# Optimization experiments

Hardware: AMD Instinct MI355X
Metric: run time of the kernel (lower is better)

The kernel has to match this reference:

```python
import jax, jax.numpy as jnp
import numpy as np

B, T, HID = 2, 1024, 1024
H, DK, DV = 16, 64, 64
K = 4            # short conv kernel size
CG = 15          # CG iterations (max_cg_step_training)
EPS = 1e-5       # norm_eps


def setup_inputs() -> dict:
    key = jax.random.key(0)
    ks = jax.random.split(key, 12)
    s = 1.0 / np.sqrt(HID)
    nrm = lambda k, sh, sc: (jax.random.normal(k, sh, jnp.float32) * sc)
    hidden_states = nrm(ks[0], (B, T, HID), 1.0)
    Wq = nrm(ks[1], (HID, HID), s)
    Wk = nrm(ks[2], (HID, HID), s)
    Wv = nrm(ks[3], (HID, HID), s)
    Wa = nrm(ks[4], (HID, H), s)
    Wb = nrm(ks[5], (HID, H), s)
    bb = jnp.zeros((H,), jnp.float32)
    A_log = jnp.log(jax.random.uniform(ks[6], (H,), jnp.float32, 1e-3, 16.0))
    dt = jnp.exp(jax.random.uniform(ks[7], (H,), jnp.float32) * (np.log(0.1) - np.log(0.001)) + np.log(0.001))
    dt = jnp.clip(dt, 1e-4)
    dt_bias = dt + jnp.log(-jnp.expm1(-dt))
    lam_init = float(np.log(np.exp(1.0 - 0.25) - 1.0))
    lambda_params = jnp.full((HID,), lam_init, jnp.float32)
    Wconv_q = nrm(ks[8], (HID, K), 0.3)
    Wconv_k = nrm(ks[9], (HID, K), 0.3)
    norm_w = jnp.ones((DV,), jnp.float32)
    Wo = nrm(ks[10], (HID, HID), s)
    return dict(hidden_states=hidden_states, Wq=Wq, Wk=Wk, Wv=Wv, Wa=Wa, Wb=Wb, bb=bb,
                A_log=A_log, dt_bias=dt_bias, lambda_params=lambda_params,
                Wconv_q=Wconv_q, Wconv_k=Wconv_k, norm_w=norm_w, Wo=Wo)


def _short_conv(x, w):
    # causal depthwise conv1d + silu. x: [b,t,c], w: [c,K]
    t = x.shape[1]
    xp = jnp.pad(x, ((0, 0), (K - 1, 0), (0, 0)))
    y = sum(xp[:, i:i + t, :] * w[:, i] for i in range(K))
    return jax.nn.silu(y)


def _l2norm(x):
    return x * jax.lax.rsqrt(jnp.sum(x * x, -1, keepdims=True) + 1e-6)


def _forward(hidden_states, Wq, Wk, Wv, Wa, Wb, bb, A_log, dt_bias, lambda_params, Wconv_q, Wconv_k, norm_w, Wo):
    b, t, _ = hidden_states.shape
    q = _short_conv(hidden_states @ Wq, Wconv_q)
    k = _short_conv(hidden_states @ Wk, Wconv_k)
    v = hidden_states @ Wv
    q = _l2norm(q.reshape(b, t, H, DK))
    k = _l2norm(k.reshape(b, t, H, DK))
    v = v.reshape(b, t, H, DV)
    beta = jax.nn.sigmoid(hidden_states @ Wb + bb)                         # [b,t,h]
    g = -jnp.exp(A_log) * jax.nn.softplus(hidden_states @ Wa + dt_bias)    # [b,t,h]
    lamb = jax.nn.softplus(lambda_params).reshape(H, DK) + 0.25            # [h,dk]

    def cg_solve(Hkk, rhs):
        # solve (Hkk + diag(lamb)) x = rhs, fixed-iteration CG, batched over [b,h]
        mv = lambda p: jnp.einsum('bhij,bhj->bhi', Hkk, p) + lamb * p
        x = jnp.zeros_like(rhs)
        r = rhs
        p = r
        rs = jnp.sum(r * r, -1, keepdims=True)
        for _ in range(CG):
            Ap = mv(p)
            alpha = rs / (jnp.sum(p * Ap, -1, keepdims=True) + 1e-12)
            x = x + alpha * p
            r = r - alpha * Ap
            rs_new = jnp.sum(r * r, -1, keepdims=True)
            p = r + (rs_new / (rs + 1e-12)) * p
            rs = rs_new
        return x

    def step(carry, inp):
        Hkk, Hkv = carry
        qt, kt, vt, gt, bt = inp
        decay = jnp.exp(gt)[..., None, None]
        w = bt[..., None, None]
        Hkk = decay * Hkk + w * (kt[..., :, None] * kt[..., None, :])
        Hkv = decay * Hkv + w * (kt[..., :, None] * vt[..., None, :])
        x = cg_solve(Hkk, qt)
        o = jnp.einsum('bhi,bhij->bhj', x, Hkv)
        return (Hkk, Hkv), o

    qT = q.transpose(1, 0, 2, 3)
    kT = k.transpose(1, 0, 2, 3)
    vT = v.transpose(1, 0, 2, 3)
    gT = g.transpose(1, 0, 2)
    bT = beta.transpose(1, 0, 2)
    Hkk0 = jnp.zeros((b, H, DK, DK), hidden_states.dtype)
    Hkv0 = jnp.zeros((b, H, DK, DV), hidden_states.dtype)
    _, oT = jax.lax.scan(jax.checkpoint(step), (Hkk0, Hkv0), (qT, kT, vT, gT, bT))
    o = oT.transpose(1, 0, 2, 3)                                           # [b,t,h,dv]
    o = o * jax.lax.rsqrt(jnp.mean(o * o, -1, keepdims=True) + EPS) * norm_w
    return o.reshape(b, t, H * DV) @ Wo


def reference(hidden_states, Wq, Wk, Wv, Wa, Wb, bb, A_log, dt_bias, lambda_params, Wconv_q, Wconv_k, norm_w, Wo):
    return _forward(hidden_states, Wq, Wk, Wv, Wa, Wb, bb, A_log, dt_bias, lambda_params, Wconv_q, Wconv_k, norm_w, Wo)
```

## Files before the change

### kernel.cpp

```cpp
#include <hip/hip_runtime.h>
#include <hip/hip_bf16.h>
#include <stdint.h>

#define T_LEN 1024
#define HIDN  1024
#define NH    16
#define DKV   64
#define KCONV 4
#define CG_IT 15
#define CC    32
#define NC    (T_LEN / CC)
#define PAD   68

typedef __attribute__((ext_vector_type(8))) short          bf16x8;
typedef __attribute__((ext_vector_type(8))) unsigned short u16x8;
typedef __attribute__((ext_vector_type(4))) unsigned short u16x4;
typedef __attribute__((ext_vector_type(4))) float          f32x4;

__device__ __forceinline__ float softplusf(float x) {
    return x > 20.f ? x : log1pf(expf(x));
}
__device__ __forceinline__ unsigned short f2bf(float x) {
    __hip_bfloat16 b = __float2bfloat16(x);
    return *reinterpret_cast<unsigned short*>(&b);
}
__device__ __forceinline__ bf16x8 pack8(float4 a, float4 b) {
    union { bf16x8 v; unsigned short u[8]; } r;
    r.u[0] = f2bf(a.x); r.u[1] = f2bf(a.y); r.u[2] = f2bf(a.z); r.u[3] = f2bf(a.w);
    r.u[4] = f2bf(b.x); r.u[5] = f2bf(b.y); r.u[6] = f2bf(b.z); r.u[7] = f2bf(b.w);
    return r.v;
}

__global__ __launch_bounds__(256) void prep(const float* __restrict__ hidden,
                                            const float* __restrict__ Wq,
                                            const float* __restrict__ Wk,
                                            const float* __restrict__ Wv,
                                            const float* __restrict__ Wo,
                                            unsigned short* __restrict__ hidden_bf,
                                            unsigned short* __restrict__ WqkvT,
                                            unsigned short* __restrict__ WoT)
{
    __shared__ unsigned short sT[64][68];
    int blk = blockIdx.x;
    int tid = threadIdx.x;
    if (blk < 2048) {
        int i = blk * 256 + tid;
        float4 v = *reinterpret_cast<const float4*>(hidden + (size_t)i * 4);
        u16x4 o;
        o.x = f2bf(v.x); o.y = f2bf(v.y); o.z = f2bf(v.z); o.w = f2bf(v.w);
        *reinterpret_cast<u16x4*>(hidden_bf + (size_t)i * 4) = o;
        return;
    }
    int r = blk - 2048;
    int m = r >> 8;
    int local = r & 255;
    int n0 = (local & 15) * 64, k0 = (local >> 4) * 64;
    const float* W = (m == 0) ? Wq : (m == 1) ? Wk : (m == 2) ? Wv : Wo;
    unsigned short* WT = (m < 3) ? (WqkvT + (size_t)m * HIDN * HIDN) : WoT;

    int rr = tid >> 4, cc4 = (tid & 15) * 4;
#pragma unroll
    for (int p = 0; p < 4; p++) {
        int rw = p * 16 + rr;
        float4 v = *reinterpret_cast<const float4*>(&W[(size_t)(k0 + rw) * HIDN + n0 + cc4]);
        sT[cc4 + 0][rw] = f2bf(v.x);
        sT[cc4 + 1][rw] = f2bf(v.y);
        sT[cc4 + 2][rw] = f2bf(v.z);
        sT[cc4 + 3][rw] = f2bf(v.w);
    }
    __syncthreads();
#pragma unroll
    for (int p = 0; p < 4; p++) {
        int rw = p * 16 + rr;
        u16x4 v = *reinterpret_cast<const u16x4*>(&sT[rw][cc4]);
        *reinterpret_cast<u16x4*>(&WT[(size_t)(n0 + rw) * HIDN + k0 + cc4]) = v;
    }
}

__global__ __launch_bounds__(256) void proj_gb(const float* __restrict__ hidden,
                                               const float* __restrict__ Wa,
                                               const float* __restrict__ Wb,
                                               const float* __restrict__ bb,
                                               const float* __restrict__ A_log,
                                               const float* __restrict__ dt_bias,
                                               float* __restrict__ g_out,
                                               float* __restrict__ beta_out)
{
    int wvid = threadIdx.x >> 6, lane = threadIdx.x & 63;
    int row = blockIdx.x * 4 + wvid;
    const float* hr = hidden + (size_t)row * HIDN;

    float da[16], db[16];
#pragma unroll
    for (int h = 0; h < 16; h++) { da[h] = 0.f; db[h] = 0.f; }

#pragma unroll 4
    for (int j = 0; j < 16; j++) {
        int i = j * 64 + lane;
        float x = hr[i];
        const float4* wa4 = reinterpret_cast<const float4*>(Wa + (size_t)i * NH);
        const float4* wb4 = reinterpret_cast<const float4*>(Wb + (size_t)i * NH);
#pragma unroll
        for (int q = 0; q < 4; q++) {
            float4 wa = wa4[q], wb = wb4[q];
            da[q * 4 + 0] += x * wa.x; da[q * 4 + 1] += x * wa.y;
            da[q * 4 + 2] += x * wa.z; da[q * 4 + 3] += x * wa.w;
            db[q * 4 + 0] += x * wb.x; db[q * 4 + 1] += x * wb.y;
            db[q * 4 + 2] += x * wb.z; db[q * 4 + 3] += x * wb.w;
        }
    }
#pragma unroll
    for (int m = 1; m < 64; m <<= 1) {
#pragma unroll
        for (int h = 0; h < 16; h++) {
            da[h] += __shfl_xor(da[h], m);
            db[h] += __shfl_xor(db[h], m);
        }
    }
    float dah = 0.f, dbh = 0.f;
#pragma unroll
    for (int h = 0; h < 16; h++) {
        bool sel = (lane == h);
        dah = sel ? da[h] : dah;
        dbh = sel ? db[h] : dbh;
    }
    if (lane < 16) {
        float sp = softplusf(dah + dt_bias[lane]);
        g_out[row * NH + lane]    = -expf(A_log[lane]) * sp;
        beta_out[row * NH + lane] = 1.f / (1.f + expf(-(dbh + bb[lane])));
    }
}

__global__ __launch_bounds__(256) void gemm_bf16(const unsigned short* __restrict__ A,
                                                 const unsigned short* __restrict__ Bt,
                                                 float* __restrict__ C,
                                                 int M, int N, int K)
{
    __shared__ unsigned short sA[64][40];
    __shared__ unsigned short sB[64][40];
    const int tid = threadIdx.x;
    const int bm = blockIdx.y * 64, bn = blockIdx.x * 64;
    const int w = tid >> 6, lane = tid & 63;
    const int l16 = lane & 15, quad = lane >> 4;
    const int lrow = tid >> 2, lk = (tid & 3) * 8;

    f32x4 acc[4];
#pragma unroll
    for (int f = 0; f < 4; f++) acc[f] = (f32x4){0.f, 0.f, 0.f, 0.f};

    const size_t arow = (size_t)(bm + lrow) * K;
    const size_t brow = (size_t)(bn + lrow) * K;

    for (int k0 = 0; k0 < K; k0 += 32) {
        u16x8 av = *reinterpret_cast<const u16x8*>(A + arow + k0 + lk);
        u16x8 bv = *reinterpret_cast<const u16x8*>(Bt + brow + k0 + lk);
        *reinterpret_cast<u16x8*>(&sA[lrow][lk]) = av;
        *reinterpret_cast<u16x8*>(&sB[lrow][lk]) = bv;
        __syncthreads();

        bf16x8 aF = *reinterpret_cast<const bf16x8*>(&sA[w * 16 + l16][quad * 8]);
#pragma unroll
        for (int f = 0; f < 4; f++) {
            bf16x8 bF = *reinterpret_cast<const bf16x8*>(&sB[f * 16 + l16][quad * 8]);
            acc[f] = __builtin_amdgcn_mfma_f32_16x16x32_bf16(aF, bF, acc[f], 0, 0, 0);
        }
        __syncthreads();
    }

#pragma unroll
    for (int f = 0; f < 4; f++) {
#pragma unroll
        for (int i = 0; i < 4; i++) {
            int m = bm + w * 16 + quad * 4 + i;
            C[(size_t)m * N + bn + f * 16 + l16] = acc[f][i];
        }
    }
}

__global__ __launch_bounds__(256) void gemm_qkv128(const unsigned short* __restrict__ A,
                                                   const unsigned short* __restrict__ Bt,
                                                   float* __restrict__ C)
{
    const int K = 1024;
    __shared__ unsigned short sA[128][40];
    __shared__ unsigned short sB[128][40];
    const int tid = threadIdx.x;
    const int bm = blockIdx.y * 128;
    const int bn = blockIdx.x * 128;
    const int w = tid >> 6, lane = tid & 63;
    const int l16 = lane & 15, quad = lane >> 4;
    const int wm = (w >> 1) * 64, wn = (w & 1) * 64;
    const int lrow = tid >> 1, lk = (tid & 1) * 16;

    f32x4 acc[4][4];
#pragma unroll
    for (int i = 0; i < 4; i++)
#pragma unroll
        for (int f = 0; f < 4; f++) acc[i][f] = (f32x4){0.f, 0.f, 0.f, 0.f};

    const size_t arow = (size_t)(bm + lrow) * K + lk;
    const size_t brow = (size_t)(bn + lrow) * K + lk;

    for (int k0 = 0; k0 < K; k0 += 32) {
        u16x8 a0 = *reinterpret_cast<const u16x8*>(A + arow + k0);
        u16x8 a1 = *reinterpret_cast<const u16x8*>(A + arow + k0 + 8);
        u16x8 b0 = *reinterpret_cast<const u16x8*>(Bt + brow + k0);
        u16x8 b1 = *reinterpret_cast<const u16x8*>(Bt + brow + k0 + 8);
        *reinterpret_cast<u16x8*>(&sA[lrow][lk])     = a0;
        *reinterpret_cast<u16x8*>(&sA[lrow][lk + 8]) = a1;
        *reinterpret_cast<u16x8*>(&sB[lrow][lk])     = b0;
        *reinterpret_cast<u16x8*>(&sB[lrow][lk + 8]) = b1;
        __syncthreads();

        bf16x8 af[4], bf[4];
#pragma unroll
        for (int i = 0; i < 4; i++)
            af[i] = *reinterpret_cast<const bf16x8*>(&sA[wm + 16 * i + l16][8 * quad]);
#pragma unroll
        for (int f = 0; f < 4; f++)
            bf[f] = *reinterpret_cast<const bf16x8*>(&sB[wn + 16 * f + l16][8 * quad]);
#pragma unroll
        for (int i = 0; i < 4; i++)
#pragma unroll
            for (int f = 0; f < 4; f++)
                acc[i][f] = __builtin_amdgcn_mfma_f32_16x16x32_bf16(af[i], bf[f], acc[i][f], 0, 0, 0);
        __syncthreads();
    }

#pragma unroll
    for (int i = 0; i < 4; i++) {
#pragma unroll
        for (int f = 0; f < 4; f++) {
            int ncol = bn + wn + 16 * f + l16;
            int mat = ncol >> 10, nc = ncol & 1023;
            float* Cb = C + (size_t)mat * (2048u * 1024u) + nc;
            int mrow = bm + wm + 16 * i + 4 * quad;
#pragma unroll
            for (int reg = 0; reg < 4; reg++)
                Cb[(size_t)(mrow + reg) * 1024] = acc[i][f][reg];
        }
    }
}

__global__ __launch_bounds__(256) void cumsum_g(const float* __restrict__ g_in,
                                                const float* __restrict__ beta_in,
                                                float* __restrict__ G_out,
                                                float* __restrict__ betaT)
{
    __shared__ float wtot[4];
    int bh = blockIdx.x;
    int b = bh >> 4, h = bh & 15;
    int tid = threadIdx.x;
    int wv = tid >> 6, lane = tid & 63;
    int t4 = tid * 4;
    size_t src = ((size_t)(b * T_LEN) + t4) * NH + h;
    float g0 = g_in[src], g1 = g_in[src + NH], g2 = g_in[src + 2 * NH], g3 = g_in[src + 3 * NH];
    float b0 = beta_in[src], b1 = beta_in[src + NH], b2 = beta_in[src + 2 * NH], b3 = beta_in[src + 3 * NH];
    float c1 = g0 + g1, c2 = c1 + g2, c3 = c2 + g3;
    float x = c3;
#pragma unroll
    for (int off = 1; off < 64; off <<= 1) {
        float y = __shfl_up(x, off);
        if (lane >= off) x += y;
    }
    float base = x - c3;
    if (lane == 63) wtot[wv] = x;
    __syncthreads();
    float woff = 0.f;
#pragma unroll
    for (int q = 0; q < 4; q++) woff += (q < wv) ? wtot[q] : 0.f;
    base += woff;
    size_t dst = (size_t)bh * T_LEN + t4;
    G_out[dst]     = base + g0;
    G_out[dst + 1] = base + c1;
    G_out[dst + 2] = base + c2;
    G_out[dst + 3] = base + c3;
    betaT[dst] = b0; betaT[dst + 1] = b1; betaT[dst + 2] = b2; betaT[dst + 3] = b3;
}

__global__ __launch_bounds__(256) void conv_silu_l2(const float* __restrict__ qpre,
                                                    const float* __restrict__ kpre,
                                                    const float* __restrict__ Wcq,
                                                    const float* __restrict__ Wck,
                                                    float* __restrict__ qbuf,
                                                    float* __restrict__ kbuf)
{
    int gidAll = blockIdx.x * 4 + (threadIdx.x >> 6);
    int which = gidAll >> 15;
    int gid = gidAll & 32767;
    const float* pre = which ? kpre : qpre;
    const float* Wc  = which ? Wck : Wcq;
    float* out       = which ? kbuf : qbuf;
    int lane = threadIdx.x & 63;
    int h = gid & 15;
    int t = (gid >> 4) & (T_LEN - 1);
    int b = gid >> 14;
    int c = h * DKV + lane;
    float acc = 0.f;
#pragma unroll
    for (int i = 0; i < KCONV; i++) {
        int ts = t - (KCONV - 1) + i;
        if (ts >= 0)
            acc += pre[((size_t)(b * T_LEN) + ts) * HIDN + c] * Wc[c * KCONV + i];
    }
    float y = acc / (1.f + expf(-acc));
    float ss = y * y;
#pragma unroll
    for (int m = 1; m < 64; m <<= 1) ss += __shfl_xor(ss, m);
    out[((size_t)(b * T_LEN) + t) * HIDN + c] = y * rsqrtf(ss + 1e-6f);
}

__global__ __launch_bounds__(256) void chunk_local(const float* __restrict__ kbuf,
                                                   const float* __restrict__ vbuf,
                                                   const float* __restrict__ G,
                                                   const float* __restrict__ betaT,
                                                   float* __restrict__ Akk,
                                                   float* __restrict__ AkvT)
{
    __shared__ float sK[CC][PAD];
    __shared__ float sV[CC][PAD];
    __shared__ float sW[CC];
    int bid = blockIdx.x;
    int half = bid & 1;
    int cidx = bid >> 1;
    int chunk = cidx & (NC - 1), bh = cidx >> 5;
    int b = bh >> 4, h = bh & 15;
    int tid = threadIdx.x;
    int i = half * 32 + (tid >> 3);
    int j0 = (tid & 7) * 8;
    int ls = tid >> 3, ld = (tid & 7) * 8;
    int t0 = chunk * CC;

    {
        size_t ga = (((size_t)(b * T_LEN) + t0 + ls) * NH + h) * 64 + ld;
        *reinterpret_cast<float4*>(&sK[ls][ld])     = *reinterpret_cast<const float4*>(&kbuf[ga]);
        *reinterpret_cast<float4*>(&sK[ls][ld + 4]) = *reinterpret_cast<const float4*>(&kbuf[ga + 4]);
        *reinterpret_cast<float4*>(&sV[ls][ld])     = *reinterpret_cast<const float4*>(&vbuf[ga]);
        *reinterpret_cast<float4*>(&sV[ls][ld + 4]) = *reinterpret_cast<const float4*>(&vbuf[ga + 4]);
        if (tid < CC) {
            float gv = G[(size_t)bh * T_LEN + t0 + tid];
            float bv = betaT[(size_t)bh * T_LEN + t0 + tid];
            float gend = __shfl(gv, 31);
            sW[tid] = expf(gend - gv) * bv;
        }
    }
    __syncthreads();

    float akk[8], akv[8];
#pragma unroll
    for (int j = 0; j < 8; j++) { akk[j] = 0.f; akv[j] = 0.f; }
#pragma unroll 4
    for (int s = 0; s < CC; s++) {
        float wk = sW[s] * sK[s][i];
        float wv = sW[s] * sV[s][i];
        float4 ka = *reinterpret_cast<const float4*>(&sK[s][j0]);
        float4 kb = *reinterpret_cast<const float4*>(&sK[s][j0 + 4]);
        akk[0] += wk * ka.x; akk[1] += wk * ka.y; akk[2] += wk * ka.z; akk[3] += wk * ka.w;
        akk[4] += wk * kb.x; akk[5] += wk * kb.y; akk[6] += wk * kb.z; akk[7] += wk * kb.w;
        akv[0] += wv * ka.x; akv[1] += wv * ka.y; akv[2] += wv * ka.z; akv[3] += wv * ka.w;
        akv[4] += wv * kb.x; akv[5] += wv * kb.y; akv[6] += wv * kb.z; akv[7] += wv * kb.w;
    }
    size_t ob = ((size_t)cidx * 64 + i) * 64 + j0;
    *reinterpret_cast<float4*>(&Akk[ob])      = make_float4(akk[0], akk[1], akk[2], akk[3]);
    *reinterpret_cast<float4*>(&Akk[ob + 4])  = make_float4(akk[4], akk[5], akk[6], akk[7]);
    *reinterpret_cast<float4*>(&AkvT[ob])     = make_float4(akv[0], akv[1], akv[2], akv[3]);
    *reinterpret_cast<float4*>(&AkvT[ob + 4]) = make_float4(akv[4], akv[5], akv[6], akv[7]);
}

__global__ __launch_bounds__(256) void chunk_prefix(const float* __restrict__ Akk,
                                                    float* __restrict__ HkvT,
                                                    const float* __restrict__ G,
                                                    unsigned short* __restrict__ Hkk_bf)
{
    __shared__ float sDec[NC];
    int blk = blockIdx.x;
    int bh = blk >> 3, sub = blk & 7;
    int tid = threadIdx.x;
    if (tid < NC)
        sDec[tid] = (tid > 0)
            ? expf(G[(size_t)bh * T_LEN + tid * CC + CC - 1] - G[(size_t)bh * T_LEN + tid * CC - 1])
            : 1.f;
    __syncthreads();
    int flat = sub * 256 + tid;
    int mat = flat >> 10, e4 = flat & 1023;
    float4 state = make_float4(0.f, 0.f, 0.f, 0.f);
    if (mat == 0) {
        const float* src = Akk + (size_t)bh * NC * 4096 + (size_t)e4 * 4;
        unsigned short* dst = Hkk_bf + (size_t)bh * NC * 4096 + (size_t)e4 * 4;
#pragma unroll 1
        for (int c0 = 0; c0 < NC; c0 += 4) {
            float4 av[4];
#pragma unroll
            for (int e = 0; e < 4; e++)
                av[e] = *reinterpret_cast<const float4*>(src + (size_t)(c0 + e) * 4096);
#pragma unroll
            for (int e = 0; e < 4; e++) {
                u16x4 o;
                o.x = f2bf(state.x); o.y = f2bf(state.y); o.z = f2bf(state.z); o.w = f2bf(state.w);
                *reinterpret_cast<u16x4*>(dst + (size_t)(c0 + e) * 4096) = o;
                float d = sDec[c0 + e];
                state.x = d * state.x + av[e].x;
                state.y = d * state.y + av[e].y;
                state.z = d * state.z + av[e].z;
                state.w = d * state.w + av[e].w;
            }
        }
    } else {
        float* base = HkvT + (size_t)bh * NC * 4096 + (size_t)e4 * 4;
#pragma unroll 1
        for (int c0 = 0; c0 < NC; c0 += 4) {
            float4 av[4];
#pragma unroll
            for (int e = 0; e < 4; e++)
                av[e] = *reinterpret_cast<const float4*>(base + (size_t)(c0 + e) * 4096);
#pragma unroll
            for (int e = 0; e < 4; e++) {
                *reinterpret_cast<float4*>(base + (size_t)(c0 + e) * 4096) = state;
                float d = sDec[c0 + e];
                state.x = d * state.x + av[e].x;
                state.y = d * state.y + av[e].y;
                state.z = d * state.z + av[e].z;
                state.w = d * state.w + av[e].w;
            }
        }
    }
}

__global__ __launch_bounds__(256, 2) void scan_mfma(
    const float* __restrict__ qbuf, const float* __restrict__ kbuf,
    const float* __restrict__ vbuf, const float* __restrict__ G,
    const float* __restrict__ betaT, const unsigned short* __restrict__ Hkk_bf,
    const float* __restrict__ HkvT0, const float* __restrict__ lambda_p,
    const float* __restrict__ norm_w, unsigned short* __restrict__ obf)
{
    __shared__ __align__(16) unsigned short sP[4][16][72];
    __shared__ __align__(16) unsigned short sM[4][16][40];

    const int tid = threadIdx.x;
    const int wv = tid >> 6, lane = tid & 63;
    const int quad = lane >> 4, l16 = lane & 15;
    const int W = blockIdx.x * 4 + wv;
    const int half = W & 1;
    const int cidx = W >> 1;
    const int bh = cidx >> 5, chunk = cidx & 31;
    const int b = bh >> 4, h = bh & 15;
    const int t0 = chunk * CC;
    const int rbofs = 16 * half + 4 * quad;
    unsigned short (*sPw)[72] = sP[wv];
    unsigned short (*sMw)[40] = sM[wv];

    const size_t rbase = ((size_t)(b * T_LEN + t0) * NH + h) * 64;
    const float* Gb = G + (size_t)bh * T_LEN + t0;
    const float* Bb = betaT + (size_t)bh * T_LEN + t0;
    const float Gprev = (chunk > 0) ? Gb[-1] : 0.f;

    float Gt[4], et[4];
#pragma unroll
    for (int reg = 0; reg < 4; reg++) {
        float g = Gb[rbofs + reg];
        Gt[reg] = g;
        et[reg] = expf(g - Gprev);
    }
    float Co[2][4];
#pragma unroll
    for (int sn = 0; sn < 2; sn++) {
        int s = 16 * sn + l16;
        float Gs = Gb[s], bts = Bb[s];
#pragma unroll
        for (int reg = 0; reg < 4; reg++) {
            int t = rbofs + reg;
            Co[sn][reg] = (s <= t) ? expf(Gt[reg] - Gs) * bts : 0.f;
        }
    }
    float lam[4], nw[4];
#pragma unroll
    for (int f = 0; f < 4; f++) {
        lam[f] = softplusf(lambda_p[h * 64 + 16 * f + l16]) + 0.25f;
        nw[f]  = norm_w[16 * f + l16];
    }

    bf16x8 Kb[2][2];
#pragma unroll
    for (int sn = 0; sn < 2; sn++) {
        const float* kr = kbuf + rbase + (size_t)(16 * sn + l16) * 1024;
#pragma unroll
        for (int ks = 0; ks < 2; ks++) {
            float4 a = *reinterpret_cast<const float4*>(kr + 8 * quad + 32 * ks);
            float4 c = *reinterpret_cast<const float4*>(kr + 8 * quad + 32 * ks + 4);
            Kb[sn][ks] = pack8(a, c);
        }
    }
    bf16x8 KTb[4];
#pragma unroll
    for (int f = 0; f < 4; f++) {
        union { bf16x8 v; unsigned short u[8]; } r;
#pragma unroll
        for (int j = 0; j < 8; j++)
            r.u[j] = f2bf(kbuf[rbase + (size_t)(8 * quad + j) * 1024 + 16 * f + l16]);
        KTb[f] = r.v;
    }
    const size_t hbase = ((size_t)(bh * NC) + chunk) * 4096;
    bf16x8 Hb[4][2];
#pragma unroll
    for (int f = 0; f < 4; f++) {
        const unsigned short* hr = Hkk_bf + hbase + (size_t)(16 * f + l16) * 64;
#pragma unroll
        for (int ks = 0; ks < 2; ks++)
            Hb[f][ks] = *reinterpret_cast<const bf16x8*>(hr + 8 * quad + 32 * ks);
    }

    f32x4 X[4], R[4], P[4];
    float rs8[4];
#pragma unroll
    for (int reg = 0; reg < 4; reg++) rs8[reg] = 0.f;
#pragma unroll
    for (int f = 0; f < 4; f++) {
#pragma unroll
        for (int reg = 0; reg < 4; reg++) {
            float q = qbuf[rbase + (size_t)(rbofs + reg) * 1024 + 16 * f + l16];
            P[f][reg] = q; R[f][reg] = q; X[f][reg] = 0.f;
            rs8[reg] += q * q;
        }
    }
#pragma unroll
    for (int reg = 0; reg < 4; reg++) {
        float v = rs8[reg];
        v += __shfl_xor(v, 1); v += __shfl_xor(v, 2);
        v += __shfl_xor(v, 4); v += __shfl_xor(v, 8);
        rs8[reg] = v;
    }

    const f32x4 zero4 = {0.f, 0.f, 0.f, 0.f};

#pragma unroll 1
    for (int it = 0; it < CG_IT; it++) {
#pragma unroll
        for (int reg = 0; reg < 4; reg++)
#pragma unroll
            for (int f = 0; f < 4; f++)
                sPw[4 * quad + reg][16 * f + l16] = f2bf(P[f][reg]);
        __threadfence_block();
        bf16x8 Pa[2];
#pragma unroll
        for (int ks = 0; ks < 2; ks++)
            Pa[ks] = *reinterpret_cast<const bf16x8*>(&sPw[l16][8 * quad + 32 * ks]);
        f32x4 D[2];
#pragma unroll
        for (int sn = 0; sn < 2; sn++) {
            f32x4 d = __builtin_amdgcn_mfma_f32_16x16x32_bf16(Pa[0], Kb[sn][0], zero4, 0, 0, 0);
            D[sn] = __builtin_amdgcn_mfma_f32_16x16x32_bf16(Pa[1], Kb[sn][1], d, 0, 0, 0);
        }
#pragma unroll
        for (int sn = 0; sn < 2; sn++)
#pragma unroll
            for (int reg = 0; reg < 4; reg++)
                sMw[4 * quad + reg][16 * sn + l16] = f2bf(Co[sn][reg] * D[sn][reg]);
        __threadfence_block();
        bf16x8 Ma = *reinterpret_cast<const bf16x8*>(&sMw[l16][8 * quad]);
        f32x4 AP[4], A2[4];
#pragma unroll
        for (int f = 0; f < 4; f++) {
            AP[f] = __builtin_amdgcn_mfma_f32_16x16x32_bf16(Ma, KTb[f], zero4, 0, 0, 0);
            f32x4 a = __builtin_amdgcn_mfma_f32_16x16x32_bf16(Pa[0], Hb[f][0], zero4, 0, 0, 0);
            A2[f] = __builtin_amdgcn_mfma_f32_16x16x32_bf16(Pa[1], Hb[f][1], a, 0, 0, 0);
        }
#pragma unroll
        for (int f = 0; f < 4; f++)
#pragma unroll
            for (int reg = 0; reg < 4; reg++)
                AP[f][reg] = lam[f] * P[f][reg] + AP[f][reg] + et[reg] * A2[f][reg];
        float alpha[4], rsn[4];
#pragma unroll
        for (int reg = 0; reg < 4; reg++) {
            float s = 0.f;
#pragma unroll
            for (int f = 0; f < 4; f++) s += P[f][reg] * AP[f][reg];
            s += __shfl_xor(s, 1); s += __shfl_xor(s, 2);
            s += __shfl_xor(s, 4); s += __shfl_xor(s, 8);
            alpha[reg] = rs8[reg] / (s + 1e-12f);
            rsn[reg] = 0.f;
        }
#pragma unroll
        for (int f = 0; f < 4; f++)
#pragma unroll
            for (int reg = 0; reg < 4; reg++) {
                X[f][reg] += alpha[reg] * P[f][reg];
                float rv = R[f][reg] - alpha[reg] * AP[f][reg];
                R[f][reg] = rv;
                rsn[reg] += rv * rv;
            }
#pragma unroll
        for (int reg = 0; reg < 4; reg++) {
            float v = rsn[reg];
            v += __shfl_xor(v, 1); v += __shfl_xor(v, 2);
            v += __shfl_xor(v, 4); v += __shfl_xor(v, 8);
            float btac = v / (rs8[reg] + 1e-12f);
            rs8[reg] = v;
#pragma unroll
            for (int f = 0; f < 4; f++)
                P[f][reg] = R[f][reg] + btac * P[f][reg];
        }
    }

#pragma unroll
    for (int reg = 0; reg < 4; reg++)
#pragma unroll
        for (int f = 0; f < 4; f++)
            sPw[4 * quad + reg][16 * f + l16] = f2bf(X[f][reg]);
    __threadfence_block();
    bf16x8 Xa[2];
#pragma unroll
    for (int ks = 0; ks < 2; ks++)
        Xa[ks] = *reinterpret_cast<const bf16x8*>(&sPw[l16][8 * quad + 32 * ks]);
    f32x4 Do[2];
#pragma unroll
    for (int sn = 0; sn < 2; sn++) {
        f32x4 d = __builtin_amdgcn_mfma_f32_16x16x32_bf16(Xa[0], Kb[sn][0], zero4, 0, 0, 0);
        Do[sn] = __builtin_amdgcn_mfma_f32_16x16x32_bf16(Xa[1], Kb[sn][1], d, 0, 0, 0);
    }
#pragma unroll
    for (int sn = 0; sn < 2; sn++)
#pragma unroll
        for (int reg = 0; reg < 4; reg++)
            sMw[4 * quad + reg][16 * sn + l16] = f2bf(Co[sn][reg] * Do[sn][reg]);
    __threadfence_block();
    bf16x8 Mo = *reinterpret_cast<const bf16x8*>(&sMw[l16][8 * quad]);
    bf16x8 Vb[4];
#pragma unroll
    for (int f = 0; f < 4; f++) {
        union { bf16x8 v; unsigned short u[8]; } r;
#pragma unroll
        for (int j = 0; j < 8; j++)
            r.u[j] = f2bf(vbuf[rbase + (size_t)(8 * quad + j) * 1024 + 16 * f + l16]);
        Vb[f] = r.v;
    }
    bf16x8 Hvb[4][2];
#pragma unroll
    for (int f = 0; f < 4; f++) {
        const float* hr = HkvT0 + hbase + (size_t)(16 * f + l16) * 64;
#pragma unroll
        for (int ks = 0; ks < 2; ks++) {
            float4 a = *reinterpret_cast<const float4*>(hr + 8 * quad + 32 * ks);
            float4 c = *reinterpret_cast<const float4*>(hr + 8 * quad + 32 * ks + 4);
            Hvb[f][ks] = pack8(a, c);
        }
    }
    f32x4 O[4];
#pragma unroll
    for (int f = 0; f < 4; f++) {
        f32x4 o1 = __builtin_amdgcn_mfma_f32_16x16x32_bf16(Mo, Vb[f], zero4, 0, 0, 0);
        f32x4 o2 = __builtin_amdgcn_mfma_f32_16x16x32_bf16(Xa[0], Hvb[f][0], zero4, 0, 0, 0);
        o2 = __builtin_amdgcn_mfma_f32_16x16x32_bf16(Xa[1], Hvb[f][1], o2, 0, 0, 0);
#pragma unroll
        for (int reg = 0; reg < 4; reg++)
            O[f][reg] = o1[reg] + et[reg] * o2[reg];
    }
#pragma unroll
    for (int reg = 0; reg < 4; reg++) {
        float s = 0.f;
#pragma unroll
        for (int f = 0; f < 4; f++) s += O[f][reg] * O[f][reg];
        s += __shfl_xor(s, 1); s += __shfl_xor(s, 2);
        s += __shfl_xor(s, 4); s += __shfl_xor(s, 8);
        float scale = rsqrtf(s * (1.f / 64.f) + 1e-5f);
        size_t orow = rbase + (size_t)(rbofs + reg) * 1024;
#pragma unroll
        for (int f = 0; f < 4; f++)
            obf[orow + 16 * f + l16] = f2bf(O[f][reg] * scale * nw[f]);
    }
}

extern "C" void kernel_launch(void* const* d_in, const int* in_sizes, int n_in,
                              void* d_out, int out_size, void* d_ws, size_t ws_size,
                              hipStream_t stream)
{
    const float* hidden   = (const float*)d_in[0];
    const float* Wq       = (const float*)d_in[1];
    const float* Wk       = (const float*)d_in[2];
    const float* Wv       = (const float*)d_in[3];
    const float* Wa       = (const float*)d_in[4];
    const float* Wb       = (const float*)d_in[5];
    const float* bb       = (const float*)d_in[6];
    const float* A_log    = (const float*)d_in[7];
    const float* dt_bias  = (const float*)d_in[8];
    const float* lambda_p = (const float*)d_in[9];
    const float* Wconv_q  = (const float*)d_in[10];
    const float* Wconv_k  = (const float*)d_in[11];
    const float* norm_w   = (const float*)d_in[12];
    const float* Wo       = (const float*)d_in[13];
    float* out = (float*)d_out;

    float* ws = (float*)d_ws;
    const size_t SZ_BIG = (size_t)2 * T_LEN * HIDN;
    float* qpre = ws;
    float* kpre = qpre + SZ_BIG;
    float* vbuf = kpre + SZ_BIG;
    float* qbuf = vbuf + SZ_BIG;
    float* kbuf = qbuf + SZ_BIG;
    float* gbuf = kbuf + SZ_BIG;
    float* bbuf = gbuf + 32768;
    float* Gbuf = bbuf + 32768;
    float* btT  = Gbuf + 32768;
    float* Akk  = btT + 32768;
    float* AkvT = Akk + (size_t)32 * NC * 4096;
    unsigned short* WoT = (unsigned short*)(AkvT + (size_t)32 * NC * 4096);

    unsigned short* hidden_bf = (unsigned short*)AkvT;
    unsigned short* WqkvT = (unsigned short*)Akk;
    unsigned short* obuf_bf = (unsigned short*)kpre;
    unsigned short* Hkk_bf = (unsigned short*)qpre;

    const int M = 2 * T_LEN;

    prep<<<3072, 256, 0, stream>>>(hidden, Wq, Wk, Wv, Wo, hidden_bf, WqkvT, WoT);
    proj_gb<<<M / 4, 256, 0, stream>>>(hidden, Wa, Wb, bb, A_log, dt_bias, gbuf, bbuf);

    dim3 gq(3 * HIDN / 128, M / 128);
    gemm_qkv128<<<gq, 256, 0, stream>>>(hidden_bf, WqkvT, qpre);
    cumsum_g<<<32, 256, 0, stream>>>(gbuf, bbuf, Gbuf, btT);
    conv_silu_l2<<<2 * M * NH / 4, 256, 0, stream>>>(qpre, kpre, Wconv_q, Wconv_k,
                                                     qbuf, kbuf);
    chunk_local<<<2048, 256, 0, stream>>>(kbuf, vbuf, Gbuf, btT, Akk, AkvT);
    chunk_prefix<<<256, 256, 0, stream>>>(Akk, AkvT, Gbuf, Hkk_bf);
    scan_mfma<<<512, 256, 0, stream>>>(qbuf, kbuf, vbuf, Gbuf, btT, Hkk_bf, AkvT,
                                       lambda_p, norm_w, obuf_bf);
    dim3 gg(HIDN / 64, M / 64);
    gemm_bf16<<<gg, 256, 0, stream>>>(obuf_bf, WoT, out, M, HIDN, HIDN);
}
```

Baseline: 251.0 us.

## Use DPP row reductions in CG scan and merge chunk_local half-blocks

Swaps the 16-lane shuffle-xor reductions in the CG scan kernel for a DPP-based reduction helper (quad_perm swaps plus row_shr 4 and row_shr 8 with bound_ctrl). It also makes each chunk_local block compute both 32-row halves of the 64x64 chunk matrices, which halves the grid and avoids loading the same K/V tile twice. The DPP path is meant to cut the ds_swizzle/permute latency on the serial CG loop. Using row_shr instead of xor masks means only some lanes hold the full row sum, so lanes that later read it may get partial sums. This is a correctness risk.

```diff
diff --git a/kernel.cpp b/kernel.cpp
--- a/kernel.cpp
+++ b/kernel.cpp
@@ -29,6 +29,15 @@
     r.u[0] = f2bf(a.x); r.u[1] = f2bf(a.y); r.u[2] = f2bf(a.z); r.u[3] = f2bf(a.w);
     r.u[4] = f2bf(b.x); r.u[5] = f2bf(b.y); r.u[6] = f2bf(b.z); r.u[7] = f2bf(b.w);
     return r.v;
+}
+
+__device__ __forceinline__ float wsum16(float x) {
+    union { float f; int i; } a, b;
+    a.f = x; b.i = __builtin_amdgcn_update_dpp(0, a.i, 0xB1, 0xF, 0xF, true); x += b.f;
+    a.f = x; b.i = __builtin_amdgcn_update_dpp(0, a.i, 0x4E, 0xF, 0xF, true); x += b.f;
+    a.f = x; b.i = __builtin_amdgcn_update_dpp(0, a.i, 0x124, 0xF, 0xF, true); x += b.f;
+    a.f = x; b.i = __builtin_amdgcn_update_dpp(0, a.i, 0x128, 0xF, 0xF, true); x += b.f;
+    return x;
 }
 
 __global__ __launch_bounds__(256) void prep(const float* __restrict__ hidden,
@@ -320,13 +329,11 @@
     __shared__ float sK[CC][PAD];
     __shared__ float sV[CC][PAD];
     __shared__ float sW[CC];
-    int bid = blockIdx.x;
-    int half = bid & 1;
-    int cidx = bid >> 1;
+    int cidx = blockIdx.x;
     int chunk = cidx & (NC - 1), bh = cidx >> 5;
     int b = bh >> 4, h = bh & 15;
     int tid = threadIdx.x;
-    int i = half * 32 + (tid >> 3);
+    int i = tid >> 3;
     int j0 = (tid & 7) * 8;
     int ls = tid >> 3, ld = (tid & 7) * 8;
     int t0 = chunk * CC;
@@ -346,25 +353,35 @@
     }
     __syncthreads();
 
-    float akk[8], akv[8];
-#pragma unroll
-    for (int j = 0; j < 8; j++) { akk[j] = 0.f; akv[j] = 0.f; }
+    float akk[2][8], akv[2][8];
+#pragma unroll
+    for (int e = 0; e < 2; e++)
+#pragma unroll
+        for (int j = 0; j < 8; j++) { akk[e][j] = 0.f; akv[e][j] = 0.f; }
 #pragma unroll 4
     for (int s = 0; s < CC; s++) {
-        float wk = sW[s] * sK[s][i];
-        float wv = sW[s] * sV[s][i];
+        float w = sW[s];
+        float wk0 = w * sK[s][i],      wv0 = w * sV[s][i];
+        float wk1 = w * sK[s][i + 32], wv1 = w * sV[s][i + 32];
         float4 ka = *reinterpret_cast<const float4*>(&sK[s][j0]);
         float4 kb = *reinterpret_cast<const float4*>(&sK[s][j0 + 4]);
-        akk[0] += wk * ka.x; akk[1] += wk * ka.y; akk[2] += wk * ka.z; akk[3] += wk * ka.w;
-        akk[4] += wk * kb.x; akk[5] += wk * kb.y; akk[6] += wk * kb.z; akk[7] += wk * kb.w;
-        akv[0] += wv * ka.x; akv[1] += wv * ka.y; akv[2] += wv * ka.z; akv[3] += wv * ka.w;
-        akv[4] += wv * kb.x; akv[5] += wv * kb.y; akv[6] += wv * kb.z; akv[7] += wv * kb.w;
-    }
-    size_t ob = ((size_t)cidx * 64 + i) * 64 + j0;
-    *reinterpret_cast<float4*>(&Akk[ob])      = make_float4(akk[0], akk[1], akk[2], akk[3]);
-    *reinterpret_cast<float4*>(&Akk[ob + 4])  = make_float4(akk[4], akk[5], akk[6], akk[7]);
-    *reinterpret_cast<float4*>(&AkvT[ob])     = make_float4(akv[0], akv[1], akv[2], akv[3]);
-    *reinterpret_cast<float4*>(&AkvT[ob + 4]) = make_float4(akv[4], akv[5], akv[6], akv[7]);
+        akk[0][0] += wk0 * ka.x; akk[0][1] += wk0 * ka.y; akk[0][2] += wk0 * ka.z; akk[0][3] += wk0 * ka.w;
+        akk[0][4] += wk0 * kb.x; akk[0][5] += wk0 * kb.y; akk[0][6] += wk0 * kb.z; akk[0][7] += wk0 * kb.w;
+        akk[1][0] += wk1 * ka.x; akk[1][1] += wk1 * ka.y; akk[1][2] += wk1 * ka.z; akk[1][3] += wk1 * ka.w;
+        akk[1][4] += wk1 * kb.x; akk[1][5] += wk1 * kb.y; akk[1][6] += wk1 * kb.z; akk[1][7] += wk1 * kb.w;
+        akv[0][0] += wv0 * ka.x; akv[0][1] += wv0 * ka.y; akv[0][2] += wv0 * ka.z; akv[0][3] += wv0 * ka.w;
+        akv[0][4] += wv0 * kb.x; akv[0][5] += wv0 * kb.y; akv[0][6] += wv0 * kb.z; akv[0][7] += wv0 * kb.w;
+        akv[1][0] += wv1 * ka.x; akv[1][1] += wv1 * ka.y; akv[1][2] += wv1 * ka.z; akv[1][3] += wv1 * ka.w;
+        akv[1][4] += wv1 * kb.x; akv[1][5] += wv1 * kb.y; akv[1][6] += wv1 * kb.z; akv[1][7] += wv1 * kb.w;
+    }
+#pragma unroll
+    for (int e = 0; e < 2; e++) {
+        size_t ob = ((size_t)cidx * 64 + i + e * 32) * 64 + j0;
+        *reinterpret_cast<float4*>(&Akk[ob])      = make_float4(akk[e][0], akk[e][1], akk[e][2], akk[e][3]);
+        *reinterpret_cast<float4*>(&Akk[ob + 4])  = make_float4(akk[e][4], akk[e][5], akk[e][6], akk[e][7]);
+        *reinterpret_cast<float4*>(&AkvT[ob])     = make_float4(akv[e][0], akv[e][1], akv[e][2], akv[e][3]);
+        *reinterpret_cast<float4*>(&AkvT[ob + 4]) = make_float4(akv[e][4], akv[e][5], akv[e][6], akv[e][7]);
+    }
 }
 
 __global__ __launch_bounds__(256) void chunk_prefix(const float* __restrict__ Akk,
@@ -523,12 +540,7 @@
         }
     }
 #pragma unroll
-    for (int reg = 0; reg < 4; reg++) {
-        float v = rs8[reg];
-        v += __shfl_xor(v, 1); v += __shfl_xor(v, 2);
-        v += __shfl_xor(v, 4); v += __shfl_xor(v, 8);
-        rs8[reg] = v;
-    }
+    for (int reg = 0; reg < 4; reg++) rs8[reg] = wsum16(rs8[reg]);
 
     const f32x4 zero4 = {0.f, 0.f, 0.f, 0.f};
 
@@ -575,8 +587,7 @@
             float s = 0.f;
 #pragma unroll
             for (int f = 0; f < 4; f++) s += P[f][reg] * AP[f][reg];
-            s += __shfl_xor(s, 1); s += __shfl_xor(s, 2);
-            s += __shfl_xor(s, 4); s += __shfl_xor(s, 8);
+            s = wsum16(s);
             alpha[reg] = rs8[reg] / (s + 1e-12f);
             rsn[reg] = 0.f;
         }
@@ -591,9 +602,7 @@
             }
 #pragma unroll
         for (int reg = 0; reg < 4; reg++) {
-            float v = rsn[reg];
-            v += __shfl_xor(v, 1); v += __shfl_xor(v, 2);
-            v += __shfl_xor(v, 4); v += __shfl_xor(v, 8);
+            float v = wsum16(rsn[reg]);
             float btac = v / (rs8[reg] + 1e-12f);
             rs8[reg] = v;
 #pragma unroll
@@ -660,8 +669,7 @@
         float s = 0.f;
 #pragma unroll
         for (int f = 0; f < 4; f++) s += O[f][reg] * O[f][reg];
-        s += __shfl_xor(s, 1); s += __shfl_xor(s, 2);
-        s += __shfl_xor(s, 4); s += __shfl_xor(s, 8);
+        s = wsum16(s);
         float scale = rsqrtf(s * (1.f / 64.f) + 1e-5f);
         size_t orow = rbase + (size_t)(rbofs + reg) * 1024;
 #pragma unroll
@@ -720,7 +728,7 @@
     cumsum_g<<<32, 256, 0, stream>>>(gbuf, bbuf, Gbuf, btT);
     conv_silu_l2<<<2 * M * NH / 4, 256, 0, stream>>>(qpre, kpre, Wconv_q, Wconv_k,
                                                      qbuf, kbuf);
-    chunk_local<<<2048, 256, 0, stream>>>(kbuf, vbuf, Gbuf, btT, Akk, AkvT);
+    chunk_local<<<1024, 256, 0, stream>>>(kbuf, vbuf, Gbuf, btT, Akk, AkvT);
     chunk_prefix<<<256, 256, 0, stream>>>(Akk, AkvT, Gbuf, Hkk_bf);
     scan_mfma<<<512, 256, 0, stream>>>(qbuf, kbuf, vbuf, Gbuf, btT, Hkk_bf, AkvT,
                                        lambda_p, norm_w, obuf_bf);
```

Measured after the change: 249.3 us. No clear change (-0.7%).
